# Optimization experiments

Measured on AMD Instinct MI355X. Metric: run time of the kernel, lower is better.

The kernel has to match this reference:

```python
import jax, jax.numpy as jnp
import numpy as np

B, H, W, C, NH, WS, NB = 8, 64, 64, 384, 12, 8, 2
N = H * W
NWT = WS * WS  # tokens per window
SHIFT = WS // 2

def _rel_index(ws):
    coords = np.stack(np.meshgrid(np.arange(ws), np.arange(ws), indexing='ij')).reshape(2, -1)
    rel = (coords[:, :, None] - coords[:, None, :]).transpose(1, 2, 0)
    rel[..., 0] += ws - 1
    rel[..., 1] += ws - 1
    rel[..., 0] *= 2 * ws - 1
    return rel.sum(-1)  # (ws*ws, ws*ws)

REL_IDX = _rel_index(WS)

def _shift_mask(h, w, ws, shift):
    img = np.zeros((h, w))
    cnt = 0
    for hs in (slice(0, -ws), slice(-ws, -shift), slice(-shift, None)):
        for wsl in (slice(0, -ws), slice(-ws, -shift), slice(-shift, None)):
            img[hs, wsl] = cnt
            cnt += 1
    win = img.reshape(h // ws, ws, w // ws, ws).transpose(0, 2, 1, 3).reshape(-1, ws * ws)
    diff = win[:, None, :] - win[:, :, None]
    return np.where(diff != 0, -100.0, 0.0).astype(np.float32)  # (nW, NWT, NWT)

MASK = jnp.asarray(_shift_mask(H, W, WS, SHIFT))

def _ln(x, g, b, eps=1e-5):
    m = jnp.mean(x, -1, keepdims=True)
    v = jnp.mean((x - m) ** 2, -1, keepdims=True)
    return (x - m) * jax.lax.rsqrt(v + eps) * g + b

def _partition(x):
    b = x.shape[0]
    x = x.reshape(b, H // WS, WS, W // WS, WS, C).transpose(0, 1, 3, 2, 4, 5)
    return x.reshape(-1, NWT, C)

def _reverse(wx, b):
    x = wx.reshape(b, H // WS, W // WS, WS, WS, C).transpose(0, 1, 3, 2, 4, 5)
    return x.reshape(b, H, W, C)

def _attention(xw, qkv_w, qkv_b, proj_w, proj_b, rpb, mask):
    B_, Nt, Cc = xw.shape
    hd = Cc // NH
    qkv = (xw @ qkv_w + qkv_b).reshape(B_, Nt, 3, NH, hd).transpose(2, 0, 3, 1, 4)
    q, k, v = qkv[0], qkv[1], qkv[2]
    bias = rpb[REL_IDX].transpose(2, 0, 1)[None]  # (1, NH, Nt, Nt)
    attn = jnp.einsum('bhnd,bhmd->bhnm', q * (hd ** -0.5), k) + bias
    if mask is not None:
        nW = mask.shape[0]
        attn = attn.reshape(B_ // nW, nW, NH, Nt, Nt) + mask[None, :, None]
        attn = attn.reshape(B_, NH, Nt, Nt)
    attn = jax.nn.softmax(attn, axis=-1)
    out = jnp.einsum('bhnm,bhmd->bhnd', attn, v).transpose(0, 2, 1, 3).reshape(B_, Nt, Cc)
    return out @ proj_w + proj_b

def _swin_block(x, p, shift):
    n1g, n1b, n2g, n2b, qw, qb, pw, pb, w1, b1, w2, b2, rpb = p
    shortcut = x
    h = _ln(x, n1g, n1b)
    if shift > 0:
        h = jnp.roll(h, (-shift, -shift), axis=(1, 2))
    hw = _attention(_partition(h), qw, qb, pw, pb, rpb, MASK if shift > 0 else None)
    h = _reverse(hw, x.shape[0])
    if shift > 0:
        h = jnp.roll(h, (shift, shift), axis=(1, 2))
    x = shortcut + h
    h = _ln(x, n2g, n2b)
    h = jax.nn.gelu(h @ w1 + b1) @ w2 + b2
    return x + h


def setup_inputs() -> dict:
    key = jax.random.key(0)
    ks = jax.random.split(key, 6)
    s = 0.02
    return {
        'x': jax.random.normal(ks[0], (B, N, C), jnp.float32),
        'outer_g': jnp.ones((NB, C), jnp.float32),
        'outer_b': jnp.zeros((NB, C), jnp.float32),
        'n1_g': jnp.ones((NB, C), jnp.float32),
        'n1_b': jnp.zeros((NB, C), jnp.float32),
        'n2_g': jnp.ones((NB, C), jnp.float32),
        'n2_b': jnp.zeros((NB, C), jnp.float32),
        'qkv_w': jax.random.normal(ks[1], (NB, C, 3 * C), jnp.float32) * s,
        'qkv_b': jnp.zeros((NB, 3 * C), jnp.float32),
        'proj_w': jax.random.normal(ks[2], (NB, C, C), jnp.float32) * s,
        'proj_b': jnp.zeros((NB, C), jnp.float32),
        'mlp_w1': jax.random.normal(ks[3], (NB, C, 4 * C), jnp.float32) * s,
        'mlp_b1': jnp.zeros((NB, 4 * C), jnp.float32),
        'mlp_w2': jax.random.normal(ks[4], (NB, 4 * C, C), jnp.float32) * s,
        'mlp_b2': jnp.zeros((NB, C), jnp.float32),
        'rpb': jax.random.normal(ks[5], (NB, (2 * WS - 1) ** 2, NH), jnp.float32) * s,
    }


def reference(x, outer_g, outer_b, n1_g, n1_b, n2_g, n2_b, qkv_w, qkv_b, proj_w, proj_b, mlp_w1, mlp_b1, mlp_w2, mlp_b2, rpb):
    xv = x.reshape(B, H, W, C)
    for i in range(NB):
        shift = 0 if i % 2 == 0 else SHIFT
        p = (n1_g[i], n1_b[i], n2_g[i], n2_b[i], qkv_w[i], qkv_b[i], proj_w[i], proj_b[i],
             mlp_w1[i], mlp_b1[i], mlp_w2[i], mlp_b2[i], rpb[i])
        residual = xv
        xv = _swin_block(_ln(xv, outer_g[i], outer_b[i]), p, shift) + residual
    return xv.reshape(B, N, C)
```

## Files before the change

### kernel.cpp

```cpp
#include <hip/hip_runtime.h>
#include <hip/hip_bf16.h>

#define BATCH 8
#define HDIM 64
#define WDIM 64
#define CC 384
#define NHE 12
#define HD 32
#define NTOK 32768
#define NBLK 2

typedef short short8 __attribute__((ext_vector_type(8)));
typedef float f32x4 __attribute__((ext_vector_type(4)));

__device__ __forceinline__ float bf2f(unsigned short u) {
  return __uint_as_float(((unsigned int)u) << 16);
}
__device__ __forceinline__ unsigned short f2bf(float f) {
  __hip_bfloat16 h = __float2bfloat16(f);
  return *reinterpret_cast<unsigned short*>(&h);
}
__device__ __forceinline__ float wave_sum(float s) {
#pragma unroll
  for (int o = 32; o; o >>= 1) s += __shfl_xor(s, o, 64);
  return s;
}
__device__ __forceinline__ float gelu_f(float x) {
  float y = 0.7978845608028654f * (x + 0.044715f * x * x * x);
  float t = 1.0f - 2.0f / (__expf(2.0f * y) + 1.0f);
  return 0.5f * x * (1.0f + t);
}
__device__ __forceinline__ int regid(int x) {
  return x < 56 ? 0 : (x < 60 ? 1 : 2);
}
__device__ __forceinline__ void gload16(const void* g, void* l) {
  __builtin_amdgcn_global_load_lds(
      (const __attribute__((address_space(1))) unsigned int*)g,
      (__attribute__((address_space(3))) unsigned int*)l, 16, 0, 0);
}

__global__ __launch_bounds__(256) void wconv_kernel(
    const float* __restrict__ src, unsigned short* __restrict__ dst, int K, int N) {
  __shared__ float tile[64 * 65];
  const int bn = blockIdx.x * 64, bk = blockIdx.y * 64;
  const int t = threadIdx.x;
  const int lk = t >> 2, ln = (t & 3) * 16;
  const float* ps = src + (size_t)(bk + lk) * N + bn + ln;
#pragma unroll
  for (int j = 0; j < 4; ++j)
    *(float4*)&tile[lk * 65 + ln + 4 * j] = *(const float4*)(ps + 4 * j);
  __syncthreads();
  const int on = t >> 2, ok = (t & 3) * 16;
  unsigned short ob[16];
#pragma unroll
  for (int j = 0; j < 16; ++j) ob[j] = f2bf(tile[(ok + j) * 65 + on]);
  uint4* pd = (uint4*)(dst + (size_t)(bn + on) * K + bk + ok);
  pd[0] = ((const uint4*)ob)[0];
  pd[1] = ((const uint4*)ob)[1];
}

__global__ __launch_bounds__(256) void bias_prep_kernel(
    const float* __restrict__ rpb, float* __restrict__ biasT) {
  int idx = blockIdx.x * 256 + threadIdx.x;
  int m = idx & 63;
  int n = (idx >> 6) & 63;
  int h = idx >> 12;
  int dr = (n >> 3) - (m >> 3) + 7;
  int dc = (n & 7) - (m & 7) + 7;
  biasT[idx] = rpb[(dr * 15 + dc) * NHE + h];
}

__global__ __launch_bounds__(256) void ln_fused_kernel(
    const float* __restrict__ xin, const float* __restrict__ og,
    const float* __restrict__ ob, const float* __restrict__ n1g,
    const float* __restrict__ n1b, float* __restrict__ y0,
    unsigned short* __restrict__ abuf, int shift) {
  const int lane = threadIdx.x & 63;
  const int token = blockIdx.x * 4 + (threadIdx.x >> 6);
  const float* px = xin + (size_t)token * CC;
  float v[6];
#pragma unroll
  for (int j = 0; j < 6; ++j) v[j] = px[j * 64 + lane];
  float s = 0.f;
#pragma unroll
  for (int j = 0; j < 6; ++j) s += v[j];
  s = wave_sum(s);
  float mean = s * (1.0f / CC);
  float q = 0.f;
#pragma unroll
  for (int j = 0; j < 6; ++j) { float d = v[j] - mean; q += d * d; }
  q = wave_sum(q);
  float rstd = rsqrtf(q * (1.0f / CC) + 1e-5f);
  float* py = y0 + (size_t)token * CC;
#pragma unroll
  for (int j = 0; j < 6; ++j) {
    int d = j * 64 + lane;
    float y = (v[j] - mean) * rstd * og[d] + ob[d];
    py[d] = y;
    v[j] = y;
  }
  s = 0.f;
#pragma unroll
  for (int j = 0; j < 6; ++j) s += v[j];
  s = wave_sum(s);
  float mean2 = s * (1.0f / CC);
  q = 0.f;
#pragma unroll
  for (int j = 0; j < 6; ++j) { float d = v[j] - mean2; q += d * d; }
  q = wave_sum(q);
  float rstd2 = rsqrtf(q * (1.0f / CC) + 1e-5f);
  int b = token >> 12;
  int hh = (token >> 6) & 63;
  int ww = token & 63;
  int r = (hh - shift) & 63;
  int c = (ww - shift) & 63;
  int wrow = (((b << 6) + ((r >> 3) << 3) + (c >> 3)) << 6) + ((r & 7) << 3) + (c & 7);
  unsigned short* pa = abuf + (size_t)wrow * CC;
#pragma unroll
  for (int j = 0; j < 6; ++j) {
    int d = j * 64 + lane;
    pa[d] = f2bf((v[j] - mean2) * rstd2 * n1g[d] + n1b[d]);
  }
}

__global__ __launch_bounds__(256) void ln2_kernel(
    const float* __restrict__ x1, const float* __restrict__ g2,
    const float* __restrict__ b2, unsigned short* __restrict__ abuf) {
  const int lane = threadIdx.x & 63;
  const int token = blockIdx.x * 4 + (threadIdx.x >> 6);
  const float* px = x1 + (size_t)token * CC;
  float v[6];
#pragma unroll
  for (int j = 0; j < 6; ++j) v[j] = px[j * 64 + lane];
  float s = 0.f;
#pragma unroll
  for (int j = 0; j < 6; ++j) s += v[j];
  s = wave_sum(s);
  float mean = s * (1.0f / CC);
  float q = 0.f;
#pragma unroll
  for (int j = 0; j < 6; ++j) { float d = v[j] - mean; q += d * d; }
  q = wave_sum(q);
  float rstd = rsqrtf(q * (1.0f / CC) + 1e-5f);
  unsigned short* pa = abuf + (size_t)token * CC;
#pragma unroll
  for (int j = 0; j < 6; ++j) {
    int d = j * 64 + lane;
    pa[d] = f2bf((v[j] - mean) * rstd * g2[d] + b2[d]);
  }
}

__global__ __launch_bounds__(256, 2) void attn_mfma_kernel(
    const unsigned short* __restrict__ qkv, const float* __restrict__ biasT,
    unsigned short* __restrict__ aout, int use_mask) {
  __shared__ char smem[55296];
  const int tid = threadIdx.x;
  const int wv = tid >> 6;
  const int lane = tid & 63;
  const int l0 = lane & 15;
  const int q = lane >> 4;
  const int wi = blockIdx.x / 3;
  const int hg = blockIdx.x - wi * 3;
  const int h = hg * 4 + wv;

  unsigned short* Pl = (unsigned short*)(smem + wv * 13824);
  unsigned short* Vt = (unsigned short*)(smem + wv * 13824 + 9216);

  const unsigned short* qbase = qkv + (size_t)(wi * 64) * 1152 + h * HD;

  short8 kf[4], qf[4];
#pragma unroll
  for (int mt = 0; mt < 4; ++mt)
    kf[mt] = *(const short8*)(qbase + (size_t)(16 * mt + l0) * 1152 + CC + 8 * q);
#pragma unroll
  for (int nt = 0; nt < 4; ++nt)
    qf[nt] = *(const short8*)(qbase + (size_t)(16 * nt + l0) * 1152 + 8 * q);

  f32x4 acc[4][4];
  const float* bh = biasT + h * 4096;
#pragma unroll
  for (int mt = 0; mt < 4; ++mt)
#pragma unroll
    for (int nt = 0; nt < 4; ++nt)
      acc[mt][nt] = *(const f32x4*)(bh + (l0 + 16 * nt) * 64 + 16 * mt + 4 * q);

  unsigned short varr[32];
  {
    const uint4* pv = (const uint4*)(qbase + (size_t)lane * 1152 + 2 * CC);
    uint4* t4 = (uint4*)varr;
    t4[0] = pv[0]; t4[1] = pv[1]; t4[2] = pv[2]; t4[3] = pv[3];
#pragma unroll
    for (int d = 0; d < 32; ++d) Vt[d * 72 + lane] = varr[d];
  }

#pragma unroll
  for (int mt = 0; mt < 4; ++mt)
#pragma unroll
    for (int nt = 0; nt < 4; ++nt)
      acc[mt][nt] = __builtin_amdgcn_mfma_f32_16x16x32_bf16(kf[mt], qf[nt], acc[mt][nt], 0, 0, 0);

  if (use_mask) {
    int wloc = wi & 63;
    int wy = (wloc >> 3) * 8, wx = (wloc & 7) * 8;
    int idn[4], idm[16];
#pragma unroll
    for (int nt = 0; nt < 4; ++nt) {
      int n = l0 + 16 * nt;
      idn[nt] = regid(wy + (n >> 3)) * 3 + regid(wx + (n & 7));
    }
#pragma unroll
    for (int mt = 0; mt < 4; ++mt)
#pragma unroll
      for (int r = 0; r < 4; ++r) {
        int m = 16 * mt + 4 * q + r;
        idm[mt * 4 + r] = regid(wy + (m >> 3)) * 3 + regid(wx + (m & 7));
      }
#pragma unroll
    for (int mt = 0; mt < 4; ++mt)
#pragma unroll
      for (int nt = 0; nt < 4; ++nt)
#pragma unroll
        for (int r = 0; r < 4; ++r)
          acc[mt][nt][r] += (idm[mt * 4 + r] == idn[nt]) ? 0.0f : -100.0f;
  }

  float mx[4], inv[4];
#pragma unroll
  for (int nt = 0; nt < 4; ++nt) {
    float m0 = -1e30f;
#pragma unroll
    for (int mt = 0; mt < 4; ++mt)
#pragma unroll
      for (int r = 0; r < 4; ++r) m0 = fmaxf(m0, acc[mt][nt][r]);
    m0 = fmaxf(m0, __shfl_xor(m0, 16, 64));
    m0 = fmaxf(m0, __shfl_xor(m0, 32, 64));
    mx[nt] = m0;
  }
#pragma unroll
  for (int nt = 0; nt < 4; ++nt) {
    float s0 = 0.f;
#pragma unroll
    for (int mt = 0; mt < 4; ++mt)
#pragma unroll
      for (int r = 0; r < 4; ++r) {
        float e = __expf(acc[mt][nt][r] - mx[nt]);
        acc[mt][nt][r] = e;
        s0 += e;
      }
    s0 += __shfl_xor(s0, 16, 64);
    s0 += __shfl_xor(s0, 32, 64);
    inv[nt] = 1.0f / s0;
  }

#pragma unroll
  for (int mt = 0; mt < 4; ++mt)
#pragma unroll
    for (int nt = 0; nt < 4; ++nt) {
      unsigned int lo = (unsigned int)f2bf(acc[mt][nt][0] * inv[nt]) |
                        ((unsigned int)f2bf(acc[mt][nt][1] * inv[nt]) << 16);
      unsigned int hi = (unsigned int)f2bf(acc[mt][nt][2] * inv[nt]) |
                        ((unsigned int)f2bf(acc[mt][nt][3] * inv[nt]) << 16);
      unsigned int* dst = (unsigned int*)(Pl + (l0 + 16 * nt) * 72 + 16 * mt + 4 * q);
      dst[0] = lo;
      dst[1] = hi;
    }
  __syncthreads();

  f32x4 oacc[4][2] = {};
#pragma unroll
  for (int kt = 0; kt < 2; ++kt) {
    short8 pa[4], vb[2];
#pragma unroll
    for (int nt = 0; nt < 4; ++nt)
      pa[nt] = *(const short8*)(Pl + (l0 + 16 * nt) * 72 + 8 * q + 32 * kt);
#pragma unroll
    for (int dt = 0; dt < 2; ++dt)
      vb[dt] = *(const short8*)(Vt + (l0 + 16 * dt) * 72 + 8 * q + 32 * kt);
#pragma unroll
    for (int nt = 0; nt < 4; ++nt)
#pragma unroll
      for (int dt = 0; dt < 2; ++dt)
        oacc[nt][dt] = __builtin_amdgcn_mfma_f32_16x16x32_bf16(pa[nt], vb[dt], oacc[nt][dt], 0, 0, 0);
  }
  __syncthreads();

  float* Ol = (float*)Pl;
#pragma unroll
  for (int nt = 0; nt < 4; ++nt)
#pragma unroll
    for (int dt = 0; dt < 2; ++dt)
#pragma unroll
      for (int r = 0; r < 4; ++r)
        Ol[(16 * nt + 4 * q + r) * 36 + l0 + 16 * dt] = oacc[nt][dt][r];
  __syncthreads();
  unsigned short ob[32];
#pragma unroll
  for (int j = 0; j < 32; ++j) ob[j] = f2bf(Ol[lane * 36 + j]);
  uint4* po = (uint4*)(aout + ((size_t)wi * 64 + lane) * CC + h * HD);
  const uint4* so = (const uint4*)ob;
  po[0] = so[0]; po[1] = so[1]; po[2] = so[2]; po[3] = so[3];
}

template <int EPI, int NN, int KK>
__global__ __launch_bounds__(256, 2) void gemm_kernel(
    const unsigned short* __restrict__ A, const unsigned short* __restrict__ Bt,
    const float* __restrict__ bias, float* __restrict__ outf,
    unsigned short* __restrict__ outb, const float* __restrict__ add0,
    const float* __restrict__ add1, int shift) {
  __shared__ __align__(1024) char smem[32768];
  unsigned short* As = (unsigned short*)smem;
  unsigned short* Bs = (unsigned short*)(smem + 16384);
  const int tid = threadIdx.x;
  const int lane = tid & 63;
  const int wv = tid >> 6;
  const int wm = wv & 1, wn = wv >> 1;
  const int rowBase = blockIdx.y * 128;
  const int colBase = blockIdx.x * 128;
  const int srow = lane >> 3;
  const int schunk = (lane & 7) ^ srow;
  const unsigned short* pA = A + (size_t)(rowBase + srow) * KK + 8 * schunk;
  const unsigned short* pB = Bt + (size_t)(colBase + srow) * KK + 8 * schunk;
  const int l0 = lane & 15;
  const int q = lane >> 4;
  f32x4 acc[4][4] = {};

  for (int k0 = 0; k0 < KK; k0 += 64) {
    __syncthreads();
#pragma unroll
    for (int i = 0; i < 4; ++i) {
      int c = i * 4 + wv;
      gload16(pA + (size_t)(8 * c) * KK + k0, (char*)As + c * 1024);
      gload16(pB + (size_t)(8 * c) * KK + k0, (char*)Bs + c * 1024);
    }
    __syncthreads();
#pragma unroll
    for (int ksub = 0; ksub < 2; ++ksub) {
      const int sc = ksub * 4 + q;
      short8 af[4], bfr[4];
#pragma unroll
      for (int im = 0; im < 4; ++im) {
        int r = wm * 64 + im * 16 + l0;
        af[im] = *(const short8*)&As[r * 64 + 8 * (sc ^ (r & 7))];
      }
#pragma unroll
      for (int in_ = 0; in_ < 4; ++in_) {
        int r = wn * 64 + in_ * 16 + l0;
        bfr[in_] = *(const short8*)&Bs[r * 64 + 8 * (sc ^ (r & 7))];
      }
#pragma unroll
      for (int im = 0; im < 4; ++im)
#pragma unroll
        for (int in_ = 0; in_ < 4; ++in_)
          acc[im][in_] = __builtin_amdgcn_mfma_f32_16x16x32_bf16(
              af[im], bfr[in_], acc[im][in_], 0, 0, 0);
    }
  }
  const int quad = lane >> 4;
  const int lc = lane & 15;
#pragma unroll
  for (int im = 0; im < 4; ++im) {
    int rb = rowBase + wm * 64 + im * 16 + quad * 4;
#pragma unroll
    for (int in_ = 0; in_ < 4; ++in_) {
      int gcol = colBase + wn * 64 + in_ * 16 + lc;
      float bv = bias[gcol];
#pragma unroll
      for (int r = 0; r < 4; ++r) {
        int grow = rb + r;
        float v = acc[im][in_][r] + bv;
        if (EPI == 0) {
          if (gcol < CC) v *= 0.17677669529663687f;
          outb[(size_t)grow * NN + gcol] = f2bf(v);
        } else if (EPI == 1) {
          outb[(size_t)grow * NN + gcol] = f2bf(gelu_f(v));
        } else if (EPI == 2) {
          int b = grow >> 12;
          int wl = (grow >> 6) & 63;
          int t = grow & 63;
          int rr = ((wl >> 3) << 3) + (t >> 3);
          int cc = ((wl & 7) << 3) + (t & 7);
          int hh2 = (rr + shift) & 63;
          int ww2 = (cc + shift) & 63;
          size_t dst = ((size_t)((b << 6) + hh2) * 64 + ww2) * CC + gcol;
          outf[dst] = add0[dst] + v;
        } else {
          size_t dst = (size_t)grow * CC + gcol;
          outf[dst] = add0[dst] + add1[dst] + v;
        }
      }
    }
  }
}

extern "C" void kernel_launch(void* const* d_in, const int* in_sizes, int n_in,
                              void* d_out, int out_size, void* d_ws, size_t ws_size,
                              hipStream_t stream) {
  const float* x    = (const float*)d_in[0];
  const float* og   = (const float*)d_in[1];
  const float* ob   = (const float*)d_in[2];
  const float* n1g  = (const float*)d_in[3];
  const float* n1b  = (const float*)d_in[4];
  const float* n2g  = (const float*)d_in[5];
  const float* n2b  = (const float*)d_in[6];
  const float* qkvw = (const float*)d_in[7];
  const float* qkvb = (const float*)d_in[8];
  const float* pw   = (const float*)d_in[9];
  const float* pb   = (const float*)d_in[10];
  const float* w1   = (const float*)d_in[11];
  const float* b1   = (const float*)d_in[12];
  const float* w2   = (const float*)d_in[13];
  const float* b2   = (const float*)d_in[14];
  const float* rpb  = (const float*)d_in[15];
  float* out = (float*)d_out;

  char* ws = (char*)d_ws;
  float* y0             = (float*)(ws);
  float* x1             = (float*)(ws + 50331648);
  unsigned short* a_bf  = (unsigned short*)(ws + 100663296);
  unsigned short* at_bf = (unsigned short*)(ws + 125829120);
  unsigned short* big_bf= (unsigned short*)(ws + 150994944);
  unsigned short* wt    = (unsigned short*)(ws + 251658240);
  float* biasT          = (float*)(ws + 150994944 + 75497472);

  for (int i = 0; i < NBLK; ++i) {
    unsigned short* wq = wt + (size_t)i * 1769472;
    wconv_kernel<<<dim3(18, 6), 256, 0, stream>>>(qkvw + (size_t)i * 442368, wq, 384, 1152);
    wconv_kernel<<<dim3(6, 6), 256, 0, stream>>>(pw + (size_t)i * 147456, wq + 442368, 384, 384);
    wconv_kernel<<<dim3(24, 6), 256, 0, stream>>>(w1 + (size_t)i * 589824, wq + 589824, 384, 1536);
    wconv_kernel<<<dim3(6, 24), 256, 0, stream>>>(w2 + (size_t)i * 589824, wq + 1179648, 1536, 384);
  }

  for (int i = 0; i < NBLK; ++i) {
    const float* xin = (i == 0) ? x : out;
    int shift = (i & 1) ? 4 : 0;
    unsigned short* wq = wt + (size_t)i * 1769472;
    ln_fused_kernel<<<8192, 256, 0, stream>>>(xin, og + i * 384, ob + i * 384,
                                              n1g + i * 384, n1b + i * 384, y0, a_bf, shift);
    gemm_kernel<0, 1152, 384><<<dim3(9, 256), 256, 0, stream>>>(
        a_bf, wq, qkvb + i * 1152, nullptr, big_bf, nullptr, nullptr, 0);
    bias_prep_kernel<<<192, 256, 0, stream>>>(rpb + i * 2700, biasT);
    attn_mfma_kernel<<<1536, 256, 0, stream>>>(big_bf, biasT, at_bf, shift ? 1 : 0);
    gemm_kernel<2, 384, 384><<<dim3(3, 256), 256, 0, stream>>>(
        at_bf, wq + 442368, pb + i * 384, x1, nullptr, y0, nullptr, shift);
    ln2_kernel<<<8192, 256, 0, stream>>>(x1, n2g + i * 384, n2b + i * 384, a_bf);
    gemm_kernel<1, 1536, 384><<<dim3(12, 256), 256, 0, stream>>>(
        a_bf, wq + 589824, b1 + i * 1536, nullptr, big_bf, nullptr, nullptr, 0);
    gemm_kernel<3, 384, 1536><<<dim3(3, 256), 256, 0, stream>>>(
        big_bf, wq + 1179648, b2 + i * 384, out, nullptr, x1, xin, 0);
  }
}
```

Baseline: 717.7 us.

## Store residual intermediates in bf16 and stream GEMM B operand from global with double-buffered A

The intermediate residual tensors y0 and x1 are now stored as bf16 instead of fp32, which halves their write and read traffic across the LN, projection-GEMM and MLP-GEMM epilogues. The GEMM kernel also stops staging the weight (B) tile in shared memory. Each wave reads its B fragments directly from global memory, and the A tile is double-buffered in LDS so the next tile's load overlaps compute, with one barrier per k-step. The trade-off is lower precision in the residual path and B reads that rely on cache hits rather than LDS reuse.

```diff
diff --git a/kernel.cpp b/kernel.cpp
--- a/kernel.cpp
+++ b/kernel.cpp
@@ -73,7 +73,7 @@
 __global__ __launch_bounds__(256) void ln_fused_kernel(
     const float* __restrict__ xin, const float* __restrict__ og,
     const float* __restrict__ ob, const float* __restrict__ n1g,
-    const float* __restrict__ n1b, float* __restrict__ y0,
+    const float* __restrict__ n1b, unsigned short* __restrict__ y0h,
     unsigned short* __restrict__ abuf, int shift) {
   const int lane = threadIdx.x & 63;
   const int token = blockIdx.x * 4 + (threadIdx.x >> 6);
@@ -91,12 +91,12 @@
   for (int j = 0; j < 6; ++j) { float d = v[j] - mean; q += d * d; }
   q = wave_sum(q);
   float rstd = rsqrtf(q * (1.0f / CC) + 1e-5f);
-  float* py = y0 + (size_t)token * CC;
+  unsigned short* py = y0h + (size_t)token * CC;
 #pragma unroll
   for (int j = 0; j < 6; ++j) {
     int d = j * 64 + lane;
     float y = (v[j] - mean) * rstd * og[d] + ob[d];
-    py[d] = y;
+    py[d] = f2bf(y);
     v[j] = y;
   }
   s = 0.f;
@@ -124,14 +124,14 @@
 }
 
 __global__ __launch_bounds__(256) void ln2_kernel(
-    const float* __restrict__ x1, const float* __restrict__ g2,
+    const unsigned short* __restrict__ x1h, const float* __restrict__ g2,
     const float* __restrict__ b2, unsigned short* __restrict__ abuf) {
   const int lane = threadIdx.x & 63;
   const int token = blockIdx.x * 4 + (threadIdx.x >> 6);
-  const float* px = x1 + (size_t)token * CC;
+  const unsigned short* px = x1h + (size_t)token * CC;
   float v[6];
 #pragma unroll
-  for (int j = 0; j < 6; ++j) v[j] = px[j * 64 + lane];
+  for (int j = 0; j < 6; ++j) v[j] = bf2f(px[j * 64 + lane]);
   float s = 0.f;
 #pragma unroll
   for (int j = 0; j < 6; ++j) s += v[j];
@@ -305,11 +305,9 @@
 __global__ __launch_bounds__(256, 2) void gemm_kernel(
     const unsigned short* __restrict__ A, const unsigned short* __restrict__ Bt,
     const float* __restrict__ bias, float* __restrict__ outf,
-    unsigned short* __restrict__ outb, const float* __restrict__ add0,
-    const float* __restrict__ add1, int shift) {
+    unsigned short* __restrict__ outb, const unsigned short* __restrict__ add0h,
+    const float* __restrict__ add1f, int shift) {
   __shared__ __align__(1024) char smem[32768];
-  unsigned short* As = (unsigned short*)smem;
-  unsigned short* Bs = (unsigned short*)(smem + 16384);
   const int tid = threadIdx.x;
   const int lane = tid & 63;
   const int wv = tid >> 6;
@@ -319,41 +317,51 @@
   const int srow = lane >> 3;
   const int schunk = (lane & 7) ^ srow;
   const unsigned short* pA = A + (size_t)(rowBase + srow) * KK + 8 * schunk;
-  const unsigned short* pB = Bt + (size_t)(colBase + srow) * KK + 8 * schunk;
   const int l0 = lane & 15;
   const int q = lane >> 4;
+  const unsigned short* pBrow[4];
+#pragma unroll
+  for (int in_ = 0; in_ < 4; ++in_)
+    pBrow[in_] = Bt + (size_t)(colBase + wn * 64 + in_ * 16 + l0) * KK + 8 * q;
   f32x4 acc[4][4] = {};
 
+#pragma unroll
+  for (int i = 0; i < 4; ++i) {
+    int c = i * 4 + wv;
+    gload16(pA + (size_t)(8 * c) * KK, smem + c * 1024);
+  }
+  int cur = 0;
   for (int k0 = 0; k0 < KK; k0 += 64) {
     __syncthreads();
-#pragma unroll
-    for (int i = 0; i < 4; ++i) {
-      int c = i * 4 + wv;
-      gload16(pA + (size_t)(8 * c) * KK + k0, (char*)As + c * 1024);
-      gload16(pB + (size_t)(8 * c) * KK + k0, (char*)Bs + c * 1024);
+    if (k0 + 64 < KK) {
+      char* nxt = smem + (cur ^ 1) * 16384;
+#pragma unroll
+      for (int i = 0; i < 4; ++i) {
+        int c = i * 4 + wv;
+        gload16(pA + (size_t)(8 * c) * KK + k0 + 64, nxt + c * 1024);
+      }
     }
-    __syncthreads();
+    const unsigned short* As = (const unsigned short*)(smem + cur * 16384);
 #pragma unroll
     for (int ksub = 0; ksub < 2; ++ksub) {
       const int sc = ksub * 4 + q;
       short8 af[4], bfr[4];
+#pragma unroll
+      for (int in_ = 0; in_ < 4; ++in_)
+        bfr[in_] = *(const short8*)(pBrow[in_] + k0 + 32 * ksub);
 #pragma unroll
       for (int im = 0; im < 4; ++im) {
         int r = wm * 64 + im * 16 + l0;
         af[im] = *(const short8*)&As[r * 64 + 8 * (sc ^ (r & 7))];
       }
 #pragma unroll
-      for (int in_ = 0; in_ < 4; ++in_) {
-        int r = wn * 64 + in_ * 16 + l0;
-        bfr[in_] = *(const short8*)&Bs[r * 64 + 8 * (sc ^ (r & 7))];
-      }
-#pragma unroll
       for (int im = 0; im < 4; ++im)
 #pragma unroll
         for (int in_ = 0; in_ < 4; ++in_)
           acc[im][in_] = __builtin_amdgcn_mfma_f32_16x16x32_bf16(
               af[im], bfr[in_], acc[im][in_], 0, 0, 0);
     }
+    cur ^= 1;
   }
   const int quad = lane >> 4;
   const int lc = lane & 15;
@@ -382,10 +390,10 @@
           int hh2 = (rr + shift) & 63;
           int ww2 = (cc + shift) & 63;
           size_t dst = ((size_t)((b << 6) + hh2) * 64 + ww2) * CC + gcol;
-          outf[dst] = add0[dst] + v;
+          outb[dst] = f2bf(bf2f(add0h[dst]) + v);
         } else {
           size_t dst = (size_t)grow * CC + gcol;
-          outf[dst] = add0[dst] + add1[dst] + v;
+          outf[dst] = bf2f(add0h[dst]) + add1f[dst] + v;
         }
       }
     }
@@ -414,13 +422,13 @@
   float* out = (float*)d_out;
 
   char* ws = (char*)d_ws;
-  float* y0             = (float*)(ws);
-  float* x1             = (float*)(ws + 50331648);
-  unsigned short* a_bf  = (unsigned short*)(ws + 100663296);
-  unsigned short* at_bf = (unsigned short*)(ws + 125829120);
-  unsigned short* big_bf= (unsigned short*)(ws + 150994944);
-  unsigned short* wt    = (unsigned short*)(ws + 251658240);
-  float* biasT          = (float*)(ws + 150994944 + 75497472);
+  unsigned short* y0h   = (unsigned short*)(ws);
+  unsigned short* x1h   = (unsigned short*)(ws + 25165824);
+  unsigned short* a_bf  = (unsigned short*)(ws + 50331648);
+  unsigned short* at_bf = (unsigned short*)(ws + 75497472);
+  unsigned short* big_bf= (unsigned short*)(ws + 100663296);
+  unsigned short* wt    = (unsigned short*)(ws + 201326592);
+  float* biasT          = (float*)(ws + 100663296 + 75497472);
 
   for (int i = 0; i < NBLK; ++i) {
     unsigned short* wq = wt + (size_t)i * 1769472;
@@ -435,17 +443,17 @@
     int shift = (i & 1) ? 4 : 0;
     unsigned short* wq = wt + (size_t)i * 1769472;
     ln_fused_kernel<<<8192, 256, 0, stream>>>(xin, og + i * 384, ob + i * 384,
-                                              n1g + i * 384, n1b + i * 384, y0, a_bf, shift);
+                                              n1g + i * 384, n1b + i * 384, y0h, a_bf, shift);
     gemm_kernel<0, 1152, 384><<<dim3(9, 256), 256, 0, stream>>>(
         a_bf, wq, qkvb + i * 1152, nullptr, big_bf, nullptr, nullptr, 0);
     bias_prep_kernel<<<192, 256, 0, stream>>>(rpb + i * 2700, biasT);
     attn_mfma_kernel<<<1536, 256, 0, stream>>>(big_bf, biasT, at_bf, shift ? 1 : 0);
     gemm_kernel<2, 384, 384><<<dim3(3, 256), 256, 0, stream>>>(
-        at_bf, wq + 442368, pb + i * 384, x1, nullptr, y0, nullptr, shift);
-    ln2_kernel<<<8192, 256, 0, stream>>>(x1, n2g + i * 384, n2b + i * 384, a_bf);
+        at_bf, wq + 442368, pb + i * 384, nullptr, x1h, y0h, nullptr, shift);
+    ln2_kernel<<<8192, 256, 0, stream>>>(x1h, n2g + i * 384, n2b + i * 384, a_bf);
     gemm_kernel<1, 1536, 384><<<dim3(12, 256), 256, 0, stream>>>(
         a_bf, wq + 589824, b1 + i * 1536, nullptr, big_bf, nullptr, nullptr, 0);
     gemm_kernel<3, 384, 1536><<<dim3(3, 256), 256, 0, stream>>>(
-        big_bf, wq + 1179648, b2 + i * 384, out, nullptr, x1, xin, 0);
-  }
-}
+        big_bf, wq + 1179648, b2 + i * 384, out, nullptr, x1h, xin, 0);
+  }
+}
```

After: 904.1 us. 1.26x slower.
